# Kernel tuning notes

Measured on AMD Instinct MI355X. Metric: run time of the kernel, lower is better.

The kernel has to match this reference:

```python
import jax, jax.numpy as jnp
import numpy as np

IN_DIM = 8192
OUT_DIM = 8192
BATCH = 2048


def setup_inputs() -> dict:
    key = jax.random.key(0)
    k1, k2, k3, k4 = jax.random.split(key, 4)
    x = jax.random.uniform(k1, (BATCH, IN_DIM), dtype=jnp.float32)  # soft bits in [0,1]
    weights = jax.random.normal(k2, (OUT_DIM, 16), dtype=jnp.float32)
    idx_a = jax.random.randint(k3, (OUT_DIM,), 0, IN_DIM, dtype=jnp.int64)
    idx_b = jax.random.randint(k4, (OUT_DIM,), 0, IN_DIM, dtype=jnp.int64)
    return {"x": x, "weights": weights, "idx_a": idx_a, "idx_b": idx_b}


def _gate_values(a, b):
    # The 16 real-valued relaxations of the 2-input binary logic gates.
    ab = a * b
    return [
        jnp.zeros_like(a),      # 0:  False
        ab,                     # 1:  a AND b
        a - ab,                 # 2:  a AND NOT b
        a,                      # 3:  a
        b - ab,                 # 4:  NOT a AND b
        b,                      # 5:  b
        a + b - 2.0 * ab,       # 6:  a XOR b
        a + b - ab,             # 7:  a OR b
        1.0 - (a + b - ab),     # 8:  NOT (a OR b)
        1.0 - (a + b - 2.0 * ab),  # 9: NOT (a XOR b)
        1.0 - b,                # 10: NOT b
        1.0 - b + ab,           # 11: a OR NOT b
        1.0 - a,                # 12: NOT a
        1.0 - a + ab,           # 13: NOT a OR b
        1.0 - ab,               # 14: NOT (a AND b)
        jnp.ones_like(a),       # 15: True
    ]


def reference(x, weights, idx_a, idx_b):
    # training=True path of LogicLayer.forward_python
    a = x[:, idx_a]  # [B, OUT]
    b = x[:, idx_b]  # [B, OUT]
    w = jax.nn.softmax(weights, axis=-1)  # [OUT, 16]
    gates = _gate_values(a, b)
    out = jnp.zeros_like(a)
    for k in range(16):  # fixed small structural loop over the 16 gates
        out = out + w[None, :, k] * gates[k]
    return out
```

## Files before the change

### kernel.cpp

```cpp
#include <hip/hip_runtime.h>
#include <hip/hip_fp16.h>

#define IN_DIM 8192
#define OUT_DIM 8192
#define BATCH 2048
#define TPB 512
#define RPB 4
#define NQ (OUT_DIM / 4 / TPB)
#define NSTG (IN_DIM / 4 / TPB)

typedef float fvec4 __attribute__((ext_vector_type(4)));

#define GLOAD_LDS16(gp, lp)                                                        \
    __builtin_amdgcn_global_load_lds(                                              \
        (const __attribute__((address_space(1))) unsigned int*)(gp),               \
        (__attribute__((address_space(3))) unsigned int*)(lp), 16, 0, 0)

#define MEMFENCE() asm volatile("" ::: "memory")

__global__ __launch_bounds__(64) void coeff_kernel(
    const float* __restrict__ w,
    const int* __restrict__ idx_a,
    const int* __restrict__ idx_b,
    int* __restrict__ pidx,
    float2* __restrict__ pcA,
    float2* __restrict__ pcB)
{
    int j = blockIdx.x * 64 + threadIdx.x;

    const float4* w4 = (const float4*)(w + (size_t)j * 16);
    float4 q0 = w4[0], q1 = w4[1], q2 = w4[2], q3 = w4[3];
    float wv[16] = { q0.x, q0.y, q0.z, q0.w,
                     q1.x, q1.y, q1.z, q1.w,
                     q2.x, q2.y, q2.z, q2.w,
                     q3.x, q3.y, q3.z, q3.w };

    float m = -1e30f;
#pragma unroll
    for (int k = 0; k < 16; ++k) m = fmaxf(m, wv[k]);
    float s = 0.f;
#pragma unroll
    for (int k = 0; k < 16; ++k) { wv[k] = __expf(wv[k] - m); s += wv[k]; }
    float inv = 1.0f / s;
#pragma unroll
    for (int k = 0; k < 16; ++k) wv[k] *= inv;

    float c0  = wv[8] + wv[9] + wv[10] + wv[11] + wv[12] + wv[13] + wv[14] + wv[15];
    float ca  = wv[2] + wv[3] + wv[6] + wv[7] - wv[8] - wv[9] - wv[12] - wv[13];
    float cb  = wv[4] + wv[5] + wv[6] + wv[7] - wv[8] - wv[9] - wv[10] - wv[11];
    float cab = wv[1] - wv[2] - wv[4] - 2.f * wv[6] - wv[7]
              + wv[8] + 2.f * wv[9] + wv[11] + wv[13] - wv[14];

    pidx[j] = ((idx_a[j] << 2) & 0xffff) | (idx_b[j] << 18);
    pcA[j]  = make_float2(c0, ca);
    pcB[j]  = make_float2(cb, cab);
}

__global__ __launch_bounds__(TPB, 4) void logic_kernel(
    const float* __restrict__ x,
    const int* __restrict__ pidx,
    const float2* __restrict__ pcA,
    const float2* __restrict__ pcB,
    float* __restrict__ out)
{
    __shared__ float xrow[2][IN_DIM];

    const int tid  = threadIdx.x;
    const int row0 = blockIdx.x * RPB;

    const int4*   pidx4 = (const int4*)pidx;
    const float4* pA4   = (const float4*)pcA;
    const float4* pB4   = (const float4*)pcB;

    int4   pi[NQ];
    float4 cA[2 * NQ];
    float4 cB[2 * NQ];
#pragma unroll
    for (int q = 0; q < NQ; ++q) {
        int j4 = q * TPB + tid;
        pi[q]         = pidx4[j4];
        cA[2 * q]     = pA4[2 * j4];
        cA[2 * q + 1] = pA4[2 * j4 + 1];
        cB[2 * q]     = pB4[2 * j4];
        cB[2 * q + 1] = pB4[2 * j4 + 1];
    }
    MEMFENCE();

    {
        const float* xr = x + (size_t)row0 * IN_DIM;
#pragma unroll
        for (int i = 0; i < NSTG; ++i)
            GLOAD_LDS16(xr + 4 * (i * TPB + tid), &xrow[0][4 * (i * TPB + tid)]);
    }
    MEMFENCE();

#pragma unroll
    for (int r = 0; r < RPB; ++r) {
        __builtin_amdgcn_s_barrier();

        if (r + 1 < RPB) {
            const float* xn = x + (size_t)(row0 + r + 1) * IN_DIM;
#pragma unroll
            for (int i = 0; i < NSTG; ++i)
                GLOAD_LDS16(xn + 4 * (i * TPB + tid), &xrow[(r + 1) & 1][4 * (i * TPB + tid)]);
        }
        MEMFENCE();

        if (r == 0 || r + 1 == RPB) asm volatile("s_waitcnt vmcnt(4)" ::: "memory");
        else                        asm volatile("s_waitcnt vmcnt(8)" ::: "memory");
        __builtin_amdgcn_s_barrier();
        MEMFENCE();

        const char* xb = (const char*)xrow[r & 1];
        fvec4* out4 = (fvec4*)(out + (size_t)(row0 + r) * OUT_DIM);

#pragma unroll
        for (int q = 0; q < NQ; ++q) {
            int4 p = pi[q];
            float a0 = *(const float*)(xb + (p.x & 0xffff)), b0 = *(const float*)(xb + ((unsigned)p.x >> 16));
            float a1 = *(const float*)(xb + (p.y & 0xffff)), b1 = *(const float*)(xb + ((unsigned)p.y >> 16));
            float a2 = *(const float*)(xb + (p.z & 0xffff)), b2 = *(const float*)(xb + ((unsigned)p.z >> 16));
            float a3 = *(const float*)(xb + (p.w & 0xffff)), b3 = *(const float*)(xb + ((unsigned)p.w >> 16));

            float4 A0 = cA[2 * q], A1 = cA[2 * q + 1];
            float4 B0 = cB[2 * q], B1 = cB[2 * q + 1];

            fvec4 o;
            o.x = fmaf(fmaf(B0.y, a0, B0.x), b0, fmaf(A0.y, a0, A0.x));
            o.y = fmaf(fmaf(B0.w, a1, B0.z), b1, fmaf(A0.w, a1, A0.z));
            o.z = fmaf(fmaf(B1.y, a2, B1.x), b2, fmaf(A1.y, a2, A1.x));
            o.w = fmaf(fmaf(B1.w, a3, B1.z), b3, fmaf(A1.w, a3, A1.z));
            __builtin_nontemporal_store(o, &out4[q * TPB + tid]);
        }
        MEMFENCE();
    }
}

extern "C" void kernel_launch(void* const* d_in, const int* in_sizes, int n_in,
                              void* d_out, int out_size, void* d_ws, size_t ws_size,
                              hipStream_t stream)
{
    const float* x       = (const float*)d_in[0];
    const float* weights = (const float*)d_in[1];
    const int*   idx_a   = (const int*)d_in[2];
    const int*   idx_b   = (const int*)d_in[3];
    float* out = (float*)d_out;

    int*    pidx = (int*)d_ws;
    float2* pcA  = (float2*)(pidx + OUT_DIM);
    float2* pcB  = pcA + OUT_DIM;

    coeff_kernel<<<OUT_DIM / 64, 64, 0, stream>>>(weights, idx_a, idx_b, pidx, pcA, pcB);
    logic_kernel<<<BATCH / RPB, TPB, 0, stream>>>(x, pidx, pcA, pcB, out);
}
```

Baseline: 117.8 us.

## Fuse softmax coefficient precompute into the logic kernel and drop the workspace

Removes the separate coeff_kernel launch and its workspace round trip. Each logic_kernel block now reads the raw weights and indices itself, then recomputes the softmax and the four polynomial coefficients for all outputs it handles. This saves a kernel launch and the dependency between the two kernels. In exchange, every block redoes the softmax work and reads roughly three times more weight bytes per block, through strided 64-byte-per-output loads, which could outweigh the launch savings.

```diff
diff --git a/kernel.cpp b/kernel.cpp
--- a/kernel.cpp
+++ b/kernel.cpp
@@ -1,5 +1,4 @@
 #include <hip/hip_runtime.h>
-#include <hip/hip_fp16.h>
 
 #define IN_DIM 8192
 #define OUT_DIM 8192
@@ -18,49 +17,11 @@
 
 #define MEMFENCE() asm volatile("" ::: "memory")
 
-__global__ __launch_bounds__(64) void coeff_kernel(
+__global__ __launch_bounds__(TPB, 4) void logic_kernel(
+    const float* __restrict__ x,
     const float* __restrict__ w,
     const int* __restrict__ idx_a,
     const int* __restrict__ idx_b,
-    int* __restrict__ pidx,
-    float2* __restrict__ pcA,
-    float2* __restrict__ pcB)
-{
-    int j = blockIdx.x * 64 + threadIdx.x;
-
-    const float4* w4 = (const float4*)(w + (size_t)j * 16);
-    float4 q0 = w4[0], q1 = w4[1], q2 = w4[2], q3 = w4[3];
-    float wv[16] = { q0.x, q0.y, q0.z, q0.w,
-                     q1.x, q1.y, q1.z, q1.w,
-                     q2.x, q2.y, q2.z, q2.w,
-                     q3.x, q3.y, q3.z, q3.w };
-
-    float m = -1e30f;
-#pragma unroll
-    for (int k = 0; k < 16; ++k) m = fmaxf(m, wv[k]);
-    float s = 0.f;
-#pragma unroll
-    for (int k = 0; k < 16; ++k) { wv[k] = __expf(wv[k] - m); s += wv[k]; }
-    float inv = 1.0f / s;
-#pragma unroll
-    for (int k = 0; k < 16; ++k) wv[k] *= inv;
-
-    float c0  = wv[8] + wv[9] + wv[10] + wv[11] + wv[12] + wv[13] + wv[14] + wv[15];
-    float ca  = wv[2] + wv[3] + wv[6] + wv[7] - wv[8] - wv[9] - wv[12] - wv[13];
-    float cb  = wv[4] + wv[5] + wv[6] + wv[7] - wv[8] - wv[9] - wv[10] - wv[11];
-    float cab = wv[1] - wv[2] - wv[4] - 2.f * wv[6] - wv[7]
-              + wv[8] + 2.f * wv[9] + wv[11] + wv[13] - wv[14];
-
-    pidx[j] = ((idx_a[j] << 2) & 0xffff) | (idx_b[j] << 18);
-    pcA[j]  = make_float2(c0, ca);
-    pcB[j]  = make_float2(cb, cab);
-}
-
-__global__ __launch_bounds__(TPB, 4) void logic_kernel(
-    const float* __restrict__ x,
-    const int* __restrict__ pidx,
-    const float2* __restrict__ pcA,
-    const float2* __restrict__ pcB,
     float* __restrict__ out)
 {
     __shared__ float xrow[2][IN_DIM];
@@ -68,29 +29,60 @@
     const int tid  = threadIdx.x;
     const int row0 = blockIdx.x * RPB;
 
-    const int4*   pidx4 = (const int4*)pidx;
-    const float4* pA4   = (const float4*)pcA;
-    const float4* pB4   = (const float4*)pcB;
-
-    int4   pi[NQ];
-    float4 cA[2 * NQ];
-    float4 cB[2 * NQ];
-#pragma unroll
-    for (int q = 0; q < NQ; ++q) {
-        int j4 = q * TPB + tid;
-        pi[q]         = pidx4[j4];
-        cA[2 * q]     = pA4[2 * j4];
-        cA[2 * q + 1] = pA4[2 * j4 + 1];
-        cB[2 * q]     = pB4[2 * j4];
-        cB[2 * q + 1] = pB4[2 * j4 + 1];
-    }
-    MEMFENCE();
-
     {
         const float* xr = x + (size_t)row0 * IN_DIM;
 #pragma unroll
         for (int i = 0; i < NSTG; ++i)
             GLOAD_LDS16(xr + 4 * (i * TPB + tid), &xrow[0][4 * (i * TPB + tid)]);
+    }
+    MEMFENCE();
+
+    int4 pi[NQ];
+#pragma unroll
+    for (int q = 0; q < NQ; ++q) {
+        int j4 = q * TPB + tid;
+        int4 ia = ((const int4*)idx_a)[j4];
+        int4 ib = ((const int4*)idx_b)[j4];
+        pi[q].x = ((ia.x << 2) & 0xffff) | (ib.x << 18);
+        pi[q].y = ((ia.y << 2) & 0xffff) | (ib.y << 18);
+        pi[q].z = ((ia.z << 2) & 0xffff) | (ib.z << 18);
+        pi[q].w = ((ia.w << 2) & 0xffff) | (ib.w << 18);
+    }
+
+    float4 cA[2 * NQ];
+    float4 cB[2 * NQ];
+#pragma unroll
+    for (int q = 0; q < NQ; ++q) {
+#pragma unroll
+        for (int k = 0; k < 4; ++k) {
+            int j = 4 * (q * TPB + tid) + k;
+            const float4* w4 = (const float4*)(w + (size_t)j * 16);
+            float4 q0 = w4[0], q1 = w4[1], q2 = w4[2], q3 = w4[3];
+            float wv[16] = { q0.x, q0.y, q0.z, q0.w,
+                             q1.x, q1.y, q1.z, q1.w,
+                             q2.x, q2.y, q2.z, q2.w,
+                             q3.x, q3.y, q3.z, q3.w };
+            float m = -1e30f;
+#pragma unroll
+            for (int t = 0; t < 16; ++t) m = fmaxf(m, wv[t]);
+            float s = 0.f;
+#pragma unroll
+            for (int t = 0; t < 16; ++t) { wv[t] = __expf(wv[t] - m); s += wv[t]; }
+            float inv = 1.0f / s;
+#pragma unroll
+            for (int t = 0; t < 16; ++t) wv[t] *= inv;
+
+            float c0  = wv[8] + wv[9] + wv[10] + wv[11] + wv[12] + wv[13] + wv[14] + wv[15];
+            float ca  = wv[2] + wv[3] + wv[6] + wv[7] - wv[8] - wv[9] - wv[12] - wv[13];
+            float cb  = wv[4] + wv[5] + wv[6] + wv[7] - wv[8] - wv[9] - wv[10] - wv[11];
+            float cab = wv[1] - wv[2] - wv[4] - 2.f * wv[6] - wv[7]
+                      + wv[8] + 2.f * wv[9] + wv[11] + wv[13] - wv[14];
+
+            if ((k & 1) == 0) { cA[2 * q + (k >> 1)].x = c0; cA[2 * q + (k >> 1)].y = ca;
+                                cB[2 * q + (k >> 1)].x = cb; cB[2 * q + (k >> 1)].y = cab; }
+            else              { cA[2 * q + (k >> 1)].z = c0; cA[2 * q + (k >> 1)].w = ca;
+                                cB[2 * q + (k >> 1)].z = cb; cB[2 * q + (k >> 1)].w = cab; }
+        }
     }
     MEMFENCE();
 
@@ -146,10 +138,5 @@
     const int*   idx_b   = (const int*)d_in[3];
     float* out = (float*)d_out;
 
-    int*    pidx = (int*)d_ws;
-    float2* pcA  = (float2*)(pidx + OUT_DIM);
-    float2* pcB  = pcA + OUT_DIM;
-
-    coeff_kernel<<<OUT_DIM / 64, 64, 0, stream>>>(weights, idx_a, idx_b, pidx, pcA, pcB);
-    logic_kernel<<<BATCH / RPB, TPB, 0, stream>>>(x, pidx, pcA, pcB, out);
+    logic_kernel<<<BATCH / RPB, TPB, 0, stream>>>(x, weights, idx_a, idx_b, out);
 }
```

After: 210.9 us. 1.79x slower.
